# Kernel tuning notes

Measured on AMD Instinct MI355X. Metric: run time of the kernel, lower is better.

The kernel has to match this reference:

```python
import jax, jax.numpy as jnp
import numpy as np

BN_EPS = 1e-5
STRIDE = 2


def setup_inputs() -> dict:
    key = jax.random.key(0)
    ks = jax.random.split(key, 8)
    B, T, Cin = 32, 1024, 128
    F, K, H = 256, 5, 512
    return {
        "x": jax.random.normal(ks[0], (B, T, Cin), jnp.float32),
        "conv_w": jax.random.normal(ks[1], (F, Cin, K), jnp.float32) * 0.05,
        "conv_b": jax.random.normal(ks[2], (F,), jnp.float32) * 0.05,
        "bn_gamma": jnp.ones((F,), jnp.float32),
        "bn_beta": jnp.zeros((F,), jnp.float32),
        "bn_mean": jnp.zeros((F,), jnp.float32),
        "bn_var": jnp.ones((F,), jnp.float32),
        "w_ih": jax.random.normal(ks[3], (4 * H, F), jnp.float32) * 0.04,
        "w_hh": jax.random.normal(ks[4], (4 * H, H), jnp.float32) * 0.04,
        "b_ih": jnp.zeros((4 * H,), jnp.float32),
        "b_hh": jnp.zeros((4 * H,), jnp.float32),
        "w_uh": jax.random.normal(ks[5], (1, H), jnp.float32) * 0.04,
        "b_uh": jnp.ones((1,), jnp.float32),
    }


def _skip_lstm(xs, w_ih, w_hh, b_ih, b_hh, w_uh, b_uh):
    # xs: [B, T', F] conv features. Skip-LSTM cell (Campos et al. Skip RNN):
    # standard LSTM + binarized state-update gate u with straight-through estimator.
    B, Tc, Fdim = xs.shape
    H = w_hh.shape[1]
    h0 = jnp.zeros((B, H), xs.dtype)
    c0 = jnp.zeros((B, H), xs.dtype)
    u0 = jnp.ones((B, 1), xs.dtype)
    # precompute input contribution to gates: [T', B, 4H]
    x_proj = jnp.einsum('btf,gf->tbg', xs, w_ih) + b_ih + b_hh

    def step(carry, xp):
        h, c, u = carry
        gates = xp + h @ w_hh.T
        i, f, g, o = jnp.split(gates, 4, axis=-1)
        c_t = jax.nn.sigmoid(f) * c + jax.nn.sigmoid(i) * jnp.tanh(g)
        h_t = jax.nn.sigmoid(o) * jnp.tanh(c_t)
        # straight-through binarization of update probability
        u_bin = u + jax.lax.stop_gradient(jnp.round(u) - u)
        c_new = u_bin * c_t + (1.0 - u_bin) * c
        h_new = u_bin * h_t + (1.0 - u_bin) * h
        du = jax.nn.sigmoid(c_new @ w_uh.T + b_uh)
        u_new = u_bin * du + (1.0 - u_bin) * (u + jnp.minimum(du, 1.0 - u))
        return (h_new, c_new, u_new), h_new

    _, hs = jax.lax.scan(step, (h0, c0, u0), x_proj)
    return jnp.swapaxes(hs, 0, 1)  # [B, T', H]


def reference(x, conv_w, conv_b, bn_gamma, bn_beta, bn_mean, bn_var,
              w_ih, w_hh, b_ih, b_hh, w_uh, b_uh):
    # Conv1d + ReLU + BatchNorm1d (eval-mode stats) on [B, Cin, T]
    xc = jnp.swapaxes(x, 1, 2)
    y = jax.lax.conv_general_dilated(
        xc, conv_w, (STRIDE,), 'VALID',
        dimension_numbers=('NCH', 'OIH', 'NCH'))
    y = jax.nn.relu(y + conv_b[None, :, None])
    inv = bn_gamma / jnp.sqrt(bn_var + BN_EPS)
    y = y * inv[None, :, None] + (bn_beta - bn_mean * inv)[None, :, None]
    y = jnp.swapaxes(y, 1, 2)  # [B, T', F]
    hs = _skip_lstm(y, w_ih, w_hh, b_ih, b_hh, w_uh, b_uh)
    return hs[:, -1, :]
```

## Files before the change

kernel.cpp:

```cpp
#include <hip/hip_runtime.h>
#include <stdint.h>
#include <math.h>

#define BB 32
#define TT 1024
#define CIN 128
#define FF 256
#define KW 5
#define HH 512
#define TP 510
#define TLAST 509
#define KC 640
#define GWG 256

#define HPK_OFF     0ull
#define PRT_OFF     262144ull
#define XP_OFF      278528ull
#define XH_OFF      (XP_OFF + 134217728ull)
#define XL_OFF      (XH_OFF + 8388608ull)
#define XSH_OFF     (XL_OFF + 8388608ull)
#define XSL_OFF     (XSH_OFF + 8388608ull)
#define WCH_OFF     (XSL_OFF + 8388608ull)
#define WCL_OFF     (WCH_OFF + 327680ull)
#define WIHH_OFF    (WCL_OFF + 327680ull)
#define WIHL_OFF    (WIHH_OFF + 1048576ull)
#define WS_NEED     (WIHL_OFF + 1048576ull)

typedef unsigned short u16;
typedef unsigned long long u64;
typedef __attribute__((ext_vector_type(8))) short short8;
typedef __attribute__((ext_vector_type(4))) float f32x4;
typedef __attribute__((ext_vector_type(4))) unsigned int u32x4;

__device__ __forceinline__ u16 f2bf(float f) {
  uint32_t u = __float_as_uint(f);
  u += 0x7fffu + ((u >> 16) & 1u);
  return (u16)(u >> 16);
}
__device__ __forceinline__ float bf2f(u16 s) { return __uint_as_float(((uint32_t)s) << 16); }
__device__ __forceinline__ void splitf(float v, u16& h, u16& l) {
  h = f2bf(v);
  l = f2bf(v - bf2f(h));
}
__device__ __forceinline__ float sigm(float x) {
  return __fdividef(1.f, 1.f + __expf(-x));
}
__device__ __forceinline__ float tanh_fast(float x) {
  float xc = fminf(x, 20.f);
  float e = __expf(2.f * xc);
  return (e - 1.f) * __fdividef(1.f, e + 1.f);
}

__global__ void prep_kernel(const float* __restrict__ x, const float* __restrict__ conv_w,
                            const float* __restrict__ w_ih,
                            u16* __restrict__ xh, u16* __restrict__ xl,
                            u16* __restrict__ wch, u16* __restrict__ wcl,
                            u16* __restrict__ wihh, u16* __restrict__ wihl) {
  int i = blockIdx.x * 256 + threadIdx.x;
  if (i < 4194304) {
    u16 h, l; splitf(x[i], h, l); xh[i] = h; xl[i] = l;
  } else if (i < 4194304 + 163840) {
    int j = i - 4194304;
    int f = j / 640, kk = j % 640;
    int c = kk & 127, k = kk >> 7;
    u16 h, l; splitf(conv_w[f * 640 + c * 5 + k], h, l);
    wch[f * 640 + kk] = h; wcl[f * 640 + kk] = l;
  } else if (i < 4194304 + 163840 + 524288) {
    int j = i - (4194304 + 163840);
    u16 h, l; splitf(w_ih[j], h, l); wihh[j] = h; wihl[j] = l;
  }
}

template <int MODE>
__global__ __launch_bounds__(256, 1) void gemm_kernel(
    const u16* __restrict__ Ah, const u16* __restrict__ Al,
    const u16* __restrict__ Bh, const u16* __restrict__ Bl,
    const float* __restrict__ e0, const float* __restrict__ e1,
    const float* __restrict__ e2, const float* __restrict__ e3, const float* __restrict__ e4,
    u16* __restrict__ outh, u16* __restrict__ outl, float* __restrict__ outf) {
  const int KDIM = (MODE == 0) ? KC : 256;
  const int MT   = (MODE == 0) ? 2 : 16;
  int bx = blockIdx.x;
  int m0 = (bx % MT) * 128;
  int n0 = (bx / MT) * 128;
  __shared__ __attribute__((aligned(16))) u16 lds[4][4096];
  int t = threadIdx.x;
  int wave = t >> 6, lane = t & 63;
  int wm = wave & 1, wn = wave >> 1;

  f32x4 acc[4][4];
#pragma unroll
  for (int i = 0; i < 4; i++)
#pragma unroll
    for (int j = 0; j < 4; j++) acc[i][j] = (f32x4){0.f, 0.f, 0.f, 0.f};

  for (int k0 = 0; k0 < KDIM; k0 += 32) {
    __syncthreads();
#pragma unroll
    for (int half = 0; half < 2; half++) {
      int e = half * 256 + t;
      int l = e & 63, tile = e >> 6;
      int kk = k0 + ((l >> 4) * 8);
      {
        int row = m0 + tile * 16 + (l & 15);
        const u16* sh = Ah + (long)row * KDIM + kk;
        const u16* sl = Al + (long)row * KDIM + kk;
        *(short8*)&lds[0][e * 8] = *(const short8*)sh;
        *(short8*)&lds[1][e * 8] = *(const short8*)sl;
      }
      {
        int n = n0 + tile * 16 + (l & 15);
        long base;
        if (MODE == 0) {
          int tp = n >> 5; if (tp > TLAST) tp = TLAST;
          base = (long)(n & 31) * 131072 + (long)tp * 256;
        } else {
          base = (long)n * 256;
        }
        *(short8*)&lds[2][e * 8] = *(const short8*)(Bh + base + kk);
        *(short8*)&lds[3][e * 8] = *(const short8*)(Bl + base + kk);
      }
    }
    __syncthreads();
    short8 af[4][2], bf[4][2];
#pragma unroll
    for (int i = 0; i < 4; i++) {
      af[i][0] = *(const short8*)&lds[0][((wm * 4 + i) * 64 + lane) * 8];
      af[i][1] = *(const short8*)&lds[1][((wm * 4 + i) * 64 + lane) * 8];
      bf[i][0] = *(const short8*)&lds[2][((wn * 4 + i) * 64 + lane) * 8];
      bf[i][1] = *(const short8*)&lds[3][((wn * 4 + i) * 64 + lane) * 8];
    }
#pragma unroll
    for (int am = 0; am < 4; am++)
#pragma unroll
      for (int an = 0; an < 4; an++) {
        acc[am][an] = __builtin_amdgcn_mfma_f32_16x16x32_bf16(af[am][0], bf[an][0], acc[am][an], 0, 0, 0);
        acc[am][an] = __builtin_amdgcn_mfma_f32_16x16x32_bf16(af[am][0], bf[an][1], acc[am][an], 0, 0, 0);
        acc[am][an] = __builtin_amdgcn_mfma_f32_16x16x32_bf16(af[am][1], bf[an][0], acc[am][an], 0, 0, 0);
      }
  }
#pragma unroll
  for (int am = 0; am < 4; am++)
#pragma unroll
    for (int an = 0; an < 4; an++) {
      int n = n0 + (wn * 4 + an) * 16 + (lane & 15);
#pragma unroll
      for (int r = 0; r < 4; r++) {
        int m = m0 + (wm * 4 + am) * 16 + (lane >> 4) * 4 + r;
        float v = acc[am][an][r];
        if (MODE == 0) {
          float inv = e1[m] / sqrtf(e4[m] + 1e-5f);
          float sh  = e2[m] - e3[m] * inv;
          v = fmaxf(v + e0[m], 0.f) * inv + sh;
          u16 h, l; splitf(v, h, l);
          outh[(long)n * 256 + m] = h;
          outl[(long)n * 256 + m] = l;
        } else {
          v += e0[m] + e1[m];
          int tp = n >> 5, b = n & 31;
          int grp = b >> 2, bb = b & 3;
          int q = m >> 9, unit = m & 511;
          int sl = unit >> 4, jjj = unit & 15;
          outf[(((long)grp * 512 + tp) * 32 + sl) * 256 + q * 64 + jjj * 4 + bb] = v;
        }
      }
    }
}

__global__ __launch_bounds__(256, 1) void scan_kernel(
    const float* __restrict__ xpg,
    const float* __restrict__ w_hh,
    const float* __restrict__ w_uh,
    const float* __restrict__ b_uh_p,
    uint32_t* __restrict__ hpk,
    u64* __restrict__ prt,
    float* __restrict__ outp)
{
  __shared__ __attribute__((aligned(16))) u16 sh_hi[4 * 528];
  __shared__ __attribute__((aligned(16))) u16 sh_lo[4 * 528];
  __shared__ float gpart[4][4][16][4];
  __shared__ float sparts[4][32];
  __shared__ int   arrive_l[32];
  __shared__ float u_l[4], ubin_l[4];
  __shared__ float wuh_l[16];
  int group = blockIdx.x & 7, slot = blockIdx.x >> 3;
  int t = threadIdx.x;
  int wave = t >> 6, lane = t & 63;
  int um = lane & 15, kq = lane >> 4;
  int nbc = um & 3;

  if (t < 16) wuh_l[t] = w_uh[slot * 16 + t];
  if (t < 4)  { u_l[t] = 1.0f; ubin_l[t] = 1.0f; }
  if (t < 32) arrive_l[t] = 0;

  short8 wfh[4][4], wfl[4][4];
#pragma unroll
  for (int q = 0; q < 4; q++) {
    long row = (long)(q * 512 + slot * 16 + um) * 512;
#pragma unroll
    for (int k4 = 0; k4 < 4; k4++) {
      union { short8 v; u16 u[8]; } Uh, Ul;
      long col0 = wave * 128 + k4 * 32 + kq * 8;
#pragma unroll
      for (int i = 0; i < 8; i++) splitf(w_hh[row + col0 + i], Uh.u[i], Ul.u[i]);
      wfh[q][k4] = Uh.v; wfl[q][k4] = Ul.v;
    }
  }
  float bu = b_uh_p[0];

  bool cell = (lane < 16);
  int  cb = wave, cj = lane;
  float c_reg = 0.f, h_reg = 0.f;

  uint32_t* hgrp = hpk + (long)group * 4096;
  u64*      pgrp = prt + (long)group * 256;

  __syncthreads();

  for (int s = 0; s < TP; s++) {
    int par = s & 1, np = par ^ 1;
    f32x4 xq;
    if (cell) {
      const float* xb = xpg + (((long)group * 512 + s) * 32 + slot) * 256;
      float x0 = xb[0 * 64 + cj * 4 + cb];
      float x1 = xb[1 * 64 + cj * 4 + cb];
      float x2 = xb[2 * 64 + cj * 4 + cb];
      float x3 = xb[3 * 64 + cj * 4 + cb];
      xq = (f32x4){x0, x1, x2, x3};
    }
    int b = t >> 6, u0 = (t & 63) * 8;
    if (s == 0) {
      *(u32x4*)&sh_hi[b * 528 + u0] = (u32x4){0u, 0u, 0u, 0u};
      *(u32x4*)&sh_lo[b * 528 + u0] = (u32x4){0u, 0u, 0u, 0u};
    } else {
      int pslot = (t & 63) >> 1;
      const u64* pw = pgrp + (long)par * 128 + b * 32 + pslot;
      const u64* hp = (const u64*)(hgrp + (long)par * 2048 + b * 512 + u0);
      uint32_t tg = (uint32_t)s;
      uint32_t e = (((uint32_t)(s - 1) >> 1) & 1u) ^ 1u;
      bool needp = ((t & 1) == 0);
      u64 v0 = __hip_atomic_load(hp,     __ATOMIC_RELAXED, __HIP_MEMORY_SCOPE_AGENT);
      u64 v1 = __hip_atomic_load(hp + 1, __ATOMIC_RELAXED, __HIP_MEMORY_SCOPE_AGENT);
      u64 v2 = __hip_atomic_load(hp + 2, __ATOMIC_RELAXED, __HIP_MEMORY_SCOPE_AGENT);
      u64 v3 = __hip_atomic_load(hp + 3, __ATOMIC_RELAXED, __HIP_MEMORY_SCOPE_AGENT);
      u64 w0 = 0;
      if (b == 0 || needp)
        w0 = __hip_atomic_load(pw, __ATOMIC_RELAXED, __HIP_MEMORY_SCOPE_AGENT);
      if (b == 0) {
        u64 w = w0;
        while ((uint32_t)(w >> 32) != tg)
          w = __hip_atomic_load(pw, __ATOMIC_RELAXED, __HIP_MEMORY_SCOPE_AGENT);
        if (needp) {
          sparts[0][pslot] = __uint_as_float((uint32_t)w);
          ((volatile int*)arrive_l)[pslot] = s;
        }
      } else {
        volatile int* arr = (volatile int*)&arrive_l[pslot];
        while (*arr != s) {}
        if (needp) {
          u64 w = w0;
          while ((uint32_t)(w >> 32) != tg)
            w = __hip_atomic_load(pw, __ATOMIC_RELAXED, __HIP_MEMORY_SCOPE_AGENT);
          sparts[b][pslot] = __uint_as_float((uint32_t)w);
        }
      }
      for (;;) {
        uint32_t bad = (((uint32_t)v0 ^ e) | ((uint32_t)(v0 >> 32) ^ e) |
                        ((uint32_t)v1 ^ e) | ((uint32_t)(v1 >> 32) ^ e) |
                        ((uint32_t)v2 ^ e) | ((uint32_t)(v2 >> 32) ^ e) |
                        ((uint32_t)v3 ^ e) | ((uint32_t)(v3 >> 32) ^ e)) & 1u;
        if (!bad) break;
        v0 = __hip_atomic_load(hp,     __ATOMIC_RELAXED, __HIP_MEMORY_SCOPE_AGENT);
        v1 = __hip_atomic_load(hp + 1, __ATOMIC_RELAXED, __HIP_MEMORY_SCOPE_AGENT);
        v2 = __hip_atomic_load(hp + 2, __ATOMIC_RELAXED, __HIP_MEMORY_SCOPE_AGENT);
        v3 = __hip_atomic_load(hp + 3, __ATOMIC_RELAXED, __HIP_MEMORY_SCOPE_AGENT);
      }
      uint32_t p[8] = {(uint32_t)v0, (uint32_t)(v0 >> 32), (uint32_t)v1, (uint32_t)(v1 >> 32),
                       (uint32_t)v2, (uint32_t)(v2 >> 32), (uint32_t)v3, (uint32_t)(v3 >> 32)};
      u32x4 hv, lv;
#pragma unroll
      for (int r = 0; r < 4; r++) {
        hv[r] = __builtin_amdgcn_perm(p[2 * r + 1], p[2 * r], 0x07060302u);
        lv[r] = __builtin_amdgcn_perm(p[2 * r + 1], p[2 * r], 0x05040100u);
      }
      *(u32x4*)&sh_hi[b * 528 + u0] = hv;
      *(u32x4*)&sh_lo[b * 528 + u0] = lv;
    }
    __syncthreads();
    if (s > 0 && t < 4) {
      float a = 0.f;
#pragma unroll
      for (int i = 0; i < 32; i++) a += sparts[t][i];
      float du = sigm(a + bu);
      float up = u_l[t], ubp = ubin_l[t];
      float un = (ubp > 0.5f) ? du : (up + fminf(du, 1.f - up));
      u_l[t] = un; ubin_l[t] = rintf(un);
    }
    f32x4 A0[4], A1[4], A2[4];
#pragma unroll
    for (int q = 0; q < 4; q++) {
      A0[q] = (f32x4){0.f, 0.f, 0.f, 0.f}; A1[q] = A0[q]; A2[q] = A0[q];
    }
#pragma unroll
    for (int k4 = 0; k4 < 4; k4++) {
      int ko = (wave * 4 + k4) * 32 + kq * 8;
      short8 bh = *(const short8*)&sh_hi[nbc * 528 + ko];
      short8 bl = *(const short8*)&sh_lo[nbc * 528 + ko];
#pragma unroll
      for (int q = 0; q < 4; q++) {
        A0[q] = __builtin_amdgcn_mfma_f32_16x16x32_bf16(wfh[q][k4], bh, A0[q], 0, 0, 0);
        A1[q] = __builtin_amdgcn_mfma_f32_16x16x32_bf16(wfh[q][k4], bl, A1[q], 0, 0, 0);
        A2[q] = __builtin_amdgcn_mfma_f32_16x16x32_bf16(wfl[q][k4], bh, A2[q], 0, 0, 0);
      }
    }
    if (um < 4) {
#pragma unroll
      for (int q = 0; q < 4; q++)
#pragma unroll
        for (int r = 0; r < 4; r++)
          gpart[wave][q][kq * 4 + r][um] = (A0[q][r] + A1[q][r]) + A2[q][r];
    }
    __syncthreads();
    if (cell) {
      float g[4];
#pragma unroll
      for (int q = 0; q < 4; q++) {
        float a = xq[q];
#pragma unroll
        for (int w = 0; w < 4; w++) a += gpart[w][q][cj][cb];
        g[q] = a;
      }
      float ig = sigm(g[0]), fg = sigm(g[1]), og = sigm(g[3]);
      float gt = tanh_fast(g[2]);
      float ct = fg * c_reg + ig * gt;
      float ht = og * tanh_fast(ct);
      bool upd = ubin_l[cb] > 0.5f;
      float cn = upd ? ct : c_reg;
      float hn = upd ? ht : h_reg;
      c_reg = cn; h_reg = hn;
      u16 hhi, hlo; splitf(hn, hhi, hlo);
      uint32_t mk = (((uint32_t)s >> 1) & 1u) ^ 1u;
      hlo = (u16)((hlo & 0xFFFEu) | mk);
      uint32_t pk = ((uint32_t)hhi << 16) | (uint32_t)hlo;
      __hip_atomic_store(hgrp + (long)np * 2048 + cb * 512 + slot * 16 + cj, pk,
                         __ATOMIC_RELAXED, __HIP_MEMORY_SCOPE_AGENT);
      float pr = cn * wuh_l[cj];
      pr += __shfl_xor(pr, 1); pr += __shfl_xor(pr, 2);
      pr += __shfl_xor(pr, 4); pr += __shfl_xor(pr, 8);
      if (s == TLAST) outp[(long)(group * 4 + cb) * 512 + slot * 16 + cj] = hn;
      if (cj == 0) {
        u64 pw = ((u64)(uint32_t)(s + 1) << 32) | (u64)__float_as_uint(pr);
        __hip_atomic_store(pgrp + (long)np * 128 + cb * 32 + slot, pw,
                           __ATOMIC_RELAXED, __HIP_MEMORY_SCOPE_AGENT);
      }
    }
  }
}

extern "C" void kernel_launch(void* const* d_in, const int* in_sizes, int n_in,
                              void* d_out, int out_size, void* d_ws, size_t ws_size,
                              hipStream_t stream) {
  const float* x      = (const float*)d_in[0];
  const float* conv_w = (const float*)d_in[1];
  const float* conv_b = (const float*)d_in[2];
  const float* gamma  = (const float*)d_in[3];
  const float* beta   = (const float*)d_in[4];
  const float* mean   = (const float*)d_in[5];
  const float* var    = (const float*)d_in[6];
  const float* w_ih   = (const float*)d_in[7];
  const float* w_hh   = (const float*)d_in[8];
  const float* b_ih   = (const float*)d_in[9];
  const float* b_hh   = (const float*)d_in[10];
  const float* w_uh   = (const float*)d_in[11];
  const float* b_uh   = (const float*)d_in[12];
  float* out = (float*)d_out;

  if (ws_size < WS_NEED) return;

  char* w = (char*)d_ws;
  uint32_t* hpk = (uint32_t*)(w + HPK_OFF);
  u64*   prt   = (u64*)(w + PRT_OFF);
  float* xp    = (float*)(w + XP_OFF);
  u16*   xh    = (u16*)(w + XH_OFF);
  u16*   xl    = (u16*)(w + XL_OFF);
  u16*   xsh   = (u16*)(w + XSH_OFF);
  u16*   xsl   = (u16*)(w + XSL_OFF);
  u16*   wch   = (u16*)(w + WCH_OFF);
  u16*   wcl   = (u16*)(w + WCL_OFF);
  u16*   wihh  = (u16*)(w + WIHH_OFF);
  u16*   wihl  = (u16*)(w + WIHL_OFF);


  prep_kernel<<<19072, 256, 0, stream>>>(x, conv_w, w_ih, xh, xl, wch, wcl, wihh, wihl);

  gemm_kernel<0><<<2 * 128, 256, 0, stream>>>(wch, wcl, xh, xl,
                                              conv_b, gamma, beta, mean, var,
                                              xsh, xsl, nullptr);
  gemm_kernel<1><<<16 * 128, 256, 0, stream>>>(wihh, wihl, xsh, xsl,
                                               b_ih, b_hh, nullptr, nullptr, nullptr,
                                               nullptr, nullptr, xp);
  scan_kernel<<<GWG, 256, 0, stream>>>(xp, w_hh, w_uh, b_uh, hpk, prt, out);
}
```

Before: 1.729 ms.

## Halve scan workgroups per group, giving each block 32 hidden units

The persistent LSTM scan now runs 16 workgroups per batch group instead of 32, each owning 32 hidden units, with two 16-unit MFMA tiles per wave and W_hh held in registers for both. The x-projection output layout, partial-sum slots and cross-block arrival flags are resized to match, and the two low-order MFMA correction products share one accumulator. The aim is to cut the number of blocks that must sync through global atomics every timestep, lowering polling and barrier latency on the serial critical path. The cost is twice the per-block MFMA work and register use per step, and fewer CUs working on the recurrence.

```diff
diff --git a/kernel.cpp b/kernel.cpp
--- a/kernel.cpp
+++ b/kernel.cpp
@@ -11,7 +11,9 @@
 #define TP 510
 #define TLAST 509
 #define KC 640
-#define GWG 256
+#define GWG 128
+#define NSLOT 16
+#define UPW 32
 
 #define HPK_OFF     0ull
 #define PRT_OFF     262144ull
@@ -160,8 +162,8 @@
           int tp = n >> 5, b = n & 31;
           int grp = b >> 2, bb = b & 3;
           int q = m >> 9, unit = m & 511;
-          int sl = unit >> 4, jjj = unit & 15;
-          outf[(((long)grp * 512 + tp) * 32 + sl) * 256 + q * 64 + jjj * 4 + bb] = v;
+          int sl = unit >> 5, jjj = unit & 31;
+          outf[(((long)grp * 512 + tp) * 16 + sl) * 512 + q * 128 + jjj * 4 + bb] = v;
         }
       }
     }
@@ -178,38 +180,40 @@
 {
   __shared__ __attribute__((aligned(16))) u16 sh_hi[4 * 528];
   __shared__ __attribute__((aligned(16))) u16 sh_lo[4 * 528];
-  __shared__ float gpart[4][4][16][4];
-  __shared__ float sparts[4][32];
-  __shared__ int   arrive_l[32];
+  __shared__ float gpart[4][4][32][5];
+  __shared__ float sparts[4][16];
+  __shared__ int   arrive_l[16];
   __shared__ float u_l[4], ubin_l[4];
-  __shared__ float wuh_l[16];
+  __shared__ float wuh_l[32];
   int group = blockIdx.x & 7, slot = blockIdx.x >> 3;
   int t = threadIdx.x;
   int wave = t >> 6, lane = t & 63;
   int um = lane & 15, kq = lane >> 4;
   int nbc = um & 3;
 
-  if (t < 16) wuh_l[t] = w_uh[slot * 16 + t];
+  if (t < 32) wuh_l[t] = w_uh[slot * 32 + t];
   if (t < 4)  { u_l[t] = 1.0f; ubin_l[t] = 1.0f; }
-  if (t < 32) arrive_l[t] = 0;
-
-  short8 wfh[4][4], wfl[4][4];
-#pragma unroll
-  for (int q = 0; q < 4; q++) {
-    long row = (long)(q * 512 + slot * 16 + um) * 512;
-#pragma unroll
-    for (int k4 = 0; k4 < 4; k4++) {
-      union { short8 v; u16 u[8]; } Uh, Ul;
-      long col0 = wave * 128 + k4 * 32 + kq * 8;
-#pragma unroll
-      for (int i = 0; i < 8; i++) splitf(w_hh[row + col0 + i], Uh.u[i], Ul.u[i]);
-      wfh[q][k4] = Uh.v; wfl[q][k4] = Ul.v;
-    }
-  }
+  if (t < 16) arrive_l[t] = 0;
+
+  short8 wfh[2][4][4], wfl[2][4][4];
+#pragma unroll
+  for (int ut = 0; ut < 2; ut++)
+#pragma unroll
+    for (int q = 0; q < 4; q++) {
+      long row = (long)(q * 512 + slot * 32 + ut * 16 + um) * 512;
+#pragma unroll
+      for (int k4 = 0; k4 < 4; k4++) {
+        union { short8 v; u16 u[8]; } Uh, Ul;
+        long col0 = wave * 128 + k4 * 32 + kq * 8;
+#pragma unroll
+        for (int i = 0; i < 8; i++) splitf(w_hh[row + col0 + i], Uh.u[i], Ul.u[i]);
+        wfh[ut][q][k4] = Uh.v; wfl[ut][q][k4] = Ul.v;
+      }
+    }
   float bu = b_uh_p[0];
 
-  bool cell = (lane < 16);
-  int  cb = wave, cj = lane;
+  bool cell = (lane < 32);
+  int  cb = wave, cj = lane & 31;
   float c_reg = 0.f, h_reg = 0.f;
 
   uint32_t* hgrp = hpk + (long)group * 4096;
@@ -221,11 +225,11 @@
     int par = s & 1, np = par ^ 1;
     f32x4 xq;
     if (cell) {
-      const float* xb = xpg + (((long)group * 512 + s) * 32 + slot) * 256;
-      float x0 = xb[0 * 64 + cj * 4 + cb];
-      float x1 = xb[1 * 64 + cj * 4 + cb];
-      float x2 = xb[2 * 64 + cj * 4 + cb];
-      float x3 = xb[3 * 64 + cj * 4 + cb];
+      const float* xb = xpg + (((long)group * 512 + s) * 16 + slot) * 512;
+      float x0 = xb[0 * 128 + cj * 4 + cb];
+      float x1 = xb[1 * 128 + cj * 4 + cb];
+      float x2 = xb[2 * 128 + cj * 4 + cb];
+      float x3 = xb[3 * 128 + cj * 4 + cb];
       xq = (f32x4){x0, x1, x2, x3};
     }
     int b = t >> 6, u0 = (t & 63) * 8;
@@ -233,12 +237,12 @@
       *(u32x4*)&sh_hi[b * 528 + u0] = (u32x4){0u, 0u, 0u, 0u};
       *(u32x4*)&sh_lo[b * 528 + u0] = (u32x4){0u, 0u, 0u, 0u};
     } else {
-      int pslot = (t & 63) >> 1;
-      const u64* pw = pgrp + (long)par * 128 + b * 32 + pslot;
+      int pslot = (t & 63) >> 2;
+      const u64* pw = pgrp + (long)par * 64 + b * 16 + pslot;
       const u64* hp = (const u64*)(hgrp + (long)par * 2048 + b * 512 + u0);
       uint32_t tg = (uint32_t)s;
       uint32_t e = (((uint32_t)(s - 1) >> 1) & 1u) ^ 1u;
-      bool needp = ((t & 1) == 0);
+      bool needp = ((t & 3) == 0);
       u64 v0 = __hip_atomic_load(hp,     __ATOMIC_RELAXED, __HIP_MEMORY_SCOPE_AGENT);
       u64 v1 = __hip_atomic_load(hp + 1, __ATOMIC_RELAXED, __HIP_MEMORY_SCOPE_AGENT);
       u64 v2 = __hip_atomic_load(hp + 2, __ATOMIC_RELAXED, __HIP_MEMORY_SCOPE_AGENT);
@@ -290,35 +294,41 @@
     if (s > 0 && t < 4) {
       float a = 0.f;
 #pragma unroll
-      for (int i = 0; i < 32; i++) a += sparts[t][i];
+      for (int i = 0; i < 16; i++) a += sparts[t][i];
       float du = sigm(a + bu);
       float up = u_l[t], ubp = ubin_l[t];
       float un = (ubp > 0.5f) ? du : (up + fminf(du, 1.f - up));
       u_l[t] = un; ubin_l[t] = rintf(un);
     }
-    f32x4 A0[4], A1[4], A2[4];
-#pragma unroll
-    for (int q = 0; q < 4; q++) {
-      A0[q] = (f32x4){0.f, 0.f, 0.f, 0.f}; A1[q] = A0[q]; A2[q] = A0[q];
-    }
+    f32x4 A0[2][4], AL[2][4];
+#pragma unroll
+    for (int ut = 0; ut < 2; ut++)
+#pragma unroll
+      for (int q = 0; q < 4; q++) {
+        A0[ut][q] = (f32x4){0.f, 0.f, 0.f, 0.f}; AL[ut][q] = A0[ut][q];
+      }
 #pragma unroll
     for (int k4 = 0; k4 < 4; k4++) {
       int ko = (wave * 4 + k4) * 32 + kq * 8;
       short8 bh = *(const short8*)&sh_hi[nbc * 528 + ko];
       short8 bl = *(const short8*)&sh_lo[nbc * 528 + ko];
 #pragma unroll
-      for (int q = 0; q < 4; q++) {
-        A0[q] = __builtin_amdgcn_mfma_f32_16x16x32_bf16(wfh[q][k4], bh, A0[q], 0, 0, 0);
-        A1[q] = __builtin_amdgcn_mfma_f32_16x16x32_bf16(wfh[q][k4], bl, A1[q], 0, 0, 0);
-        A2[q] = __builtin_amdgcn_mfma_f32_16x16x32_bf16(wfl[q][k4], bh, A2[q], 0, 0, 0);
-      }
+      for (int ut = 0; ut < 2; ut++)
+#pragma unroll
+        for (int q = 0; q < 4; q++) {
+          A0[ut][q] = __builtin_amdgcn_mfma_f32_16x16x32_bf16(wfh[ut][q][k4], bh, A0[ut][q], 0, 0, 0);
+          AL[ut][q] = __builtin_amdgcn_mfma_f32_16x16x32_bf16(wfh[ut][q][k4], bl, AL[ut][q], 0, 0, 0);
+          AL[ut][q] = __builtin_amdgcn_mfma_f32_16x16x32_bf16(wfl[ut][q][k4], bh, AL[ut][q], 0, 0, 0);
+        }
     }
     if (um < 4) {
 #pragma unroll
-      for (int q = 0; q < 4; q++)
-#pragma unroll
-        for (int r = 0; r < 4; r++)
-          gpart[wave][q][kq * 4 + r][um] = (A0[q][r] + A1[q][r]) + A2[q][r];
+      for (int ut = 0; ut < 2; ut++)
+#pragma unroll
+        for (int q = 0; q < 4; q++)
+#pragma unroll
+          for (int r = 0; r < 4; r++)
+            gpart[wave][q][ut * 16 + kq * 4 + r][um] = A0[ut][q][r] + AL[ut][q][r];
     }
     __syncthreads();
     if (cell) {
@@ -342,15 +352,16 @@
       uint32_t mk = (((uint32_t)s >> 1) & 1u) ^ 1u;
       hlo = (u16)((hlo & 0xFFFEu) | mk);
       uint32_t pk = ((uint32_t)hhi << 16) | (uint32_t)hlo;
-      __hip_atomic_store(hgrp + (long)np * 2048 + cb * 512 + slot * 16 + cj, pk,
+      __hip_atomic_store(hgrp + (long)np * 2048 + cb * 512 + slot * 32 + cj, pk,
                          __ATOMIC_RELAXED, __HIP_MEMORY_SCOPE_AGENT);
       float pr = cn * wuh_l[cj];
       pr += __shfl_xor(pr, 1); pr += __shfl_xor(pr, 2);
       pr += __shfl_xor(pr, 4); pr += __shfl_xor(pr, 8);
-      if (s == TLAST) outp[(long)(group * 4 + cb) * 512 + slot * 16 + cj] = hn;
+      pr += __shfl_xor(pr, 16);
+      if (s == TLAST) outp[(long)(group * 4 + cb) * 512 + slot * 32 + cj] = hn;
       if (cj == 0) {
         u64 pw = ((u64)(uint32_t)(s + 1) << 32) | (u64)__float_as_uint(pr);
-        __hip_atomic_store(pgrp + (long)np * 128 + cb * 32 + slot, pw,
+        __hip_atomic_store(pgrp + (long)np * 64 + cb * 16 + slot, pw,
                            __ATOMIC_RELAXED, __HIP_MEMORY_SCOPE_AGENT);
       }
     }
```

Result: slower. 1.947 ms (+12.6%).
